# Kernel tuning notes

Measured on AMD Instinct MI355X. Metric: run time of the kernel, lower is better.

The kernel has to match this reference:

```python
import jax, jax.numpy as jnp
import numpy as np

EPS = 1e-08

def quantize_weights(w):
    # absmean ternary quantization: round(w/delta) clipped to {-1,0,1}, rescaled by delta
    delta = jnp.mean(jnp.abs(w)) + EPS
    w_quant = jnp.clip(jnp.round(w / delta), -1.0, 1.0)
    return w_quant * delta

def setup_inputs() -> dict:
    key = jax.random.key(0)
    k1, k2 = jax.random.split(key)
    B, T, IN, OUT = 8, 16, 4096, 11008
    x = jax.random.normal(k1, (B, T, IN), dtype=jnp.float32)
    weight = jax.random.normal(k2, (OUT, IN), dtype=jnp.float32)
    bias = jnp.zeros((OUT,), dtype=jnp.float32)
    return {"x": x, "weight": weight, "bias": bias}

def reference(x, weight, bias):
    w_quant = quantize_weights(weight)
    # F.linear: x @ w_quant.T + bias
    out = jnp.einsum("bti,oi->bto", x, w_quant) + bias
    return out
```

## Files before the change

### kernel.cpp

```cpp
#include <hip/hip_runtime.h>
#include <hip/hip_bf16.h>

typedef __bf16 bf16x8 __attribute__((ext_vector_type(8)));
typedef float f32x4 __attribute__((ext_vector_type(4)));
typedef unsigned short ushort8 __attribute__((ext_vector_type(8)));
typedef unsigned short ushort4v __attribute__((ext_vector_type(4)));

constexpr int M = 128;
constexpr int K = 4096;
constexpr int N = 11008;
constexpr int BN = 64;
constexpr int BK = 32;
constexpr int KSPLIT = 4;
constexpr int KBLK = K / KSPLIT;
constexpr int NBX = N / BN;
constexpr long long NW = (long long)N * K;
constexpr int RBLK = 2048;
constexpr size_t MN = (size_t)M * N;

constexpr size_t PART_OFF = 0;
constexpr size_t XBF_OFF  = 8192;
constexpr size_t P_OFF    = XBF_OFF + (size_t)M * K * 2;
constexpr size_t WS_NEED  = P_OFF + KSPLIT * MN * sizeof(float);
constexpr size_t WS_MIN   = RBLK * sizeof(float);

__device__ __forceinline__ unsigned short f2bf_bits(float f) {
    unsigned int u = __builtin_bit_cast(unsigned int, f);
    u += 0x7FFFu + ((u >> 16) & 1u);
    return (unsigned short)(u >> 16);
}

template <bool CVT>
__global__ __launch_bounds__(256) void absmean_partial(const float* __restrict__ w,
                                                       const float* __restrict__ x,
                                                       float* __restrict__ partials,
                                                       unsigned short* __restrict__ xbf)
{
    const int gtid = blockIdx.x * blockDim.x + threadIdx.x;
    if (CVT && gtid < M * K / 8) {
        const float4* xp = (const float4*)x + (size_t)gtid * 2;
        float4 a = xp[0], b = xp[1];
        ushort8 o;
        o[0] = f2bf_bits(a.x); o[1] = f2bf_bits(a.y);
        o[2] = f2bf_bits(a.z); o[3] = f2bf_bits(a.w);
        o[4] = f2bf_bits(b.x); o[5] = f2bf_bits(b.y);
        o[6] = f2bf_bits(b.z); o[7] = f2bf_bits(b.w);
        *(ushort8*)(xbf + (size_t)gtid * 8) = o;
    }
    const int n4 = (int)(NW / 4);
    const float4* w4 = (const float4*)w;
    float s0 = 0.f, s1 = 0.f, s2 = 0.f, s3 = 0.f;
    for (int i = gtid; i < n4; i += gridDim.x * blockDim.x) {
        float4 v = w4[i];
        s0 += fabsf(v.x); s1 += fabsf(v.y); s2 += fabsf(v.z); s3 += fabsf(v.w);
    }
    float s = (s0 + s1) + (s2 + s3);
#pragma unroll
    for (int off = 32; off > 0; off >>= 1) s += __shfl_down(s, off, 64);
    __shared__ float red[4];
    if ((threadIdx.x & 63) == 0) red[threadIdx.x >> 6] = s;
    __syncthreads();
    if (threadIdx.x == 0)
        partials[blockIdx.x] = (red[0] + red[1]) + (red[2] + red[3]);
}

template <int KSTEPS, bool PRE>
__global__ __launch_bounds__(256, 4) void bitlinear_gemm(
    const void* __restrict__ Xsrc, const float* __restrict__ W,
    const float* __restrict__ bias, const float* __restrict__ partials,
    float* __restrict__ dbase)
{
    constexpr int LDSW = 40;
    __shared__ __attribute__((aligned(16))) unsigned short xs[2][M * LDSW];
    __shared__ __attribute__((aligned(16))) unsigned short wsm[2][BN * LDSW];
    __shared__ float red[4];

    const int tid = threadIdx.x;
    const int lane = tid & 63;
    const int wid = tid >> 6;
    const int wm = wid >> 1;
    const int wn = wid & 1;
    const int cgrp = lane >> 4;
    const int l15 = lane & 15;
    const int n0 = blockIdx.x * BN;
    const int kk0 = PRE ? blockIdx.y * KBLK : 0;
    const int K4 = K / 4;

    const unsigned short* xb = (const unsigned short*)Xsrc;
    const float4* x4p = (const float4*)Xsrc;
    const float4* w4p = (const float4*)W;

    ushort8 xrA[2], xrB[2];
    float4 xfA[4], xfB[4];
    float4 wrA[2], wrB[2];

    auto issue_set = [&](int t, ushort8 (&xr)[2], float4 (&xf)[4], float4 (&wr)[2]) {
        if constexpr (PRE) {
#pragma unroll
            for (int i = 0; i < 2; ++i) {
                const int j = tid + i * 256;
                xr[i] = *(const ushort8*)(xb + (size_t)(j >> 2) * K + kk0 + t * BK + (j & 3) * 8);
            }
        } else {
#pragma unroll
            for (int i = 0; i < 4; ++i) {
                const int j = tid + i * 256;
                xf[i] = x4p[(size_t)(j >> 3) * K4 + (t * BK) / 4 + (j & 7)];
            }
        }
#pragma unroll
        for (int i = 0; i < 2; ++i) {
            const int j = tid + i * 256;
            wr[i] = w4p[(size_t)(n0 + (j >> 3)) * K4 + (kk0 + t * BK) / 4 + (j & 7)];
        }
    };

    float ps[RBLK / 256];
#pragma unroll
    for (int i = 0; i < RBLK / 256; ++i) ps[i] = partials[tid + i * 256];

    issue_set(0, xrA, xfA, wrA);
    if (KSTEPS > 1) issue_set(1, xrB, xfB, wrB);

    float s = 0.f;
#pragma unroll
    for (int i = 0; i < RBLK / 256; ++i) s += ps[i];
#pragma unroll
    for (int off = 32; off > 0; off >>= 1) s += __shfl_down(s, off, 64);
    if (lane == 0) red[wid] = s;
    __syncthreads();
    const float delta =
        (float)((double)((red[0] + red[1]) + (red[2] + red[3])) / (double)NW + 1e-8);
    const float inv_delta = 1.0f / delta;

    auto stage_set = [&](int buf, ushort8 (&xr)[2], float4 (&xf)[4], float4 (&wr)[2]) {
        if constexpr (PRE) {
#pragma unroll
            for (int i = 0; i < 2; ++i) {
                const int j = tid + i * 256;
                *(ushort8*)&xs[buf][(j >> 2) * LDSW + (j & 3) * 8] = xr[i];
            }
        } else {
#pragma unroll
            for (int i = 0; i < 4; ++i) {
                const int j = tid + i * 256;
                float4 v = xf[i];
                ushort4v o;
                o[0] = f2bf_bits(v.x); o[1] = f2bf_bits(v.y);
                o[2] = f2bf_bits(v.z); o[3] = f2bf_bits(v.w);
                *(ushort4v*)&xs[buf][(j >> 3) * LDSW + (j & 7) * 4] = o;
            }
        }
#pragma unroll
        for (int i = 0; i < 2; ++i) {
            const int j = tid + i * 256;
            float wf[4] = {wr[i].x, wr[i].y, wr[i].z, wr[i].w};
            ushort4v wq;
#pragma unroll
            for (int e = 0; e < 4; ++e) {
                float qv = rintf(wf[e] * inv_delta);
                qv = fminf(1.f, fmaxf(-1.f, qv));
                wq[e] = f2bf_bits(qv);
            }
            *(ushort4v*)&wsm[buf][(j >> 3) * LDSW + (j & 7) * 4] = wq;
        }
    };

    f32x4 acc[4][2] = {};

    auto compute = [&](int buf) {
        const unsigned short* xcur = xs[buf];
        const unsigned short* wcur = wsm[buf];
        bf16x8 afr[4], bfr[2];
#pragma unroll
        for (int f = 0; f < 4; ++f)
            afr[f] = *(const bf16x8*)&xcur[(wm * 64 + f * 16 + l15) * LDSW + cgrp * 8];
#pragma unroll
        for (int g = 0; g < 2; ++g)
            bfr[g] = *(const bf16x8*)&wcur[(wn * 32 + g * 16 + l15) * LDSW + cgrp * 8];
#pragma unroll
        for (int f = 0; f < 4; ++f)
#pragma unroll
            for (int g = 0; g < 2; ++g)
                acc[f][g] = __builtin_amdgcn_mfma_f32_16x16x32_bf16(
                    afr[f], bfr[g], acc[f][g], 0, 0, 0);
    };

    for (int t = 0; t < KSTEPS; t += 2) {
        stage_set(0, xrA, xfA, wrA);
        if (t + 2 < KSTEPS) issue_set(t + 2, xrA, xfA, wrA);
        __syncthreads();
        compute(0);
        stage_set(1, xrB, xfB, wrB);
        if (t + 3 < KSTEPS) issue_set(t + 3, xrB, xfB, wrB);
        __syncthreads();
        compute(1);
    }

    float* dst = PRE ? dbase + (size_t)blockIdx.y * MN : dbase;
#pragma unroll
    for (int f = 0; f < 4; ++f) {
        const int mrow = wm * 64 + f * 16 + cgrp * 4;
#pragma unroll
        for (int g = 0; g < 2; ++g) {
            const int ocol = n0 + wn * 32 + g * 16 + l15;
            const float bv = PRE ? 0.f : bias[ocol];
#pragma unroll
            for (int r = 0; r < 4; ++r)
                dst[(size_t)(mrow + r) * N + ocol] = delta * acc[f][g][r] + bv;
        }
    }
}

__global__ __launch_bounds__(256) void combine(const float* __restrict__ p,
                                               const float* __restrict__ bias,
                                               float4* __restrict__ out)
{
    const int i4 = blockIdx.x * blockDim.x + threadIdx.x;
    constexpr int N4 = N / 4;
    if (i4 >= (int)(MN / 4)) return;
    const int col4 = i4 % N4;
    float4 s = *(const float4*)(bias + col4 * 4);
#pragma unroll
    for (int y = 0; y < KSPLIT; ++y) {
        float4 v = ((const float4*)(p + y * MN))[i4];
        s.x += v.x; s.y += v.y; s.z += v.z; s.w += v.w;
    }
    out[i4] = s;
}

extern "C" void kernel_launch(void* const* d_in, const int* in_sizes, int n_in,
                              void* d_out, int out_size, void* d_ws, size_t ws_size,
                              hipStream_t stream) {
    const float* x = (const float*)d_in[0];
    const float* w = (const float*)d_in[1];
    const float* bias = (const float*)d_in[2];
    float* out = (float*)d_out;
    float* partials = (float*)((char*)d_ws + PART_OFF);
    unsigned short* xbf = (unsigned short*)((char*)d_ws + XBF_OFF);
    float* pbase = (float*)((char*)d_ws + P_OFF);

    if (ws_size >= WS_NEED) {
        absmean_partial<true><<<RBLK, 256, 0, stream>>>(w, x, partials, xbf);
        bitlinear_gemm<KBLK / BK, true><<<dim3(NBX, KSPLIT), 256, 0, stream>>>(
            xbf, w, bias, partials, pbase);
        combine<<<(int)(MN / 4 + 255) / 256, 256, 0, stream>>>(pbase, bias, (float4*)out);
    } else if (ws_size >= WS_MIN) {
        absmean_partial<false><<<RBLK, 256, 0, stream>>>(w, x, partials, xbf);
        bitlinear_gemm<K / BK, false><<<dim3(NBX, 1), 256, 0, stream>>>(
            x, w, bias, partials, out);
    }
}
```

Before: 71.67 us.

## Fuse split-K combine into GEMM via per-column-tile atomic ticket

Drops the separate combine kernel. Each split-K GEMM block takes a ticket with an atomic counter per N tile, and the last block to finish sums the partial slices plus bias into the output for that tile. This saves a kernel launch and lets the reduction overlap with other blocks' GEMM work, and the partials are more likely to still be in cache. In exchange it adds a memset launch and thread fences, and the final reduction is serialized onto one block per tile.

```diff
diff --git a/kernel.cpp b/kernel.cpp
--- a/kernel.cpp
+++ b/kernel.cpp
@@ -19,7 +19,8 @@
 constexpr size_t MN = (size_t)M * N;
 
 constexpr size_t PART_OFF = 0;
-constexpr size_t XBF_OFF  = 8192;
+constexpr size_t DONE_OFF = 8192;
+constexpr size_t XBF_OFF  = 16384;
 constexpr size_t P_OFF    = XBF_OFF + (size_t)M * K * 2;
 constexpr size_t WS_NEED  = P_OFF + KSPLIT * MN * sizeof(float);
 constexpr size_t WS_MIN   = RBLK * sizeof(float);
@@ -68,7 +69,8 @@
 __global__ __launch_bounds__(256, 4) void bitlinear_gemm(
     const void* __restrict__ Xsrc, const float* __restrict__ W,
     const float* __restrict__ bias, const float* __restrict__ partials,
-    float* __restrict__ dbase)
+    float* __restrict__ dbase, float* __restrict__ outp,
+    unsigned int* __restrict__ done)
 {
     constexpr int LDSW = 40;
     __shared__ __attribute__((aligned(16))) unsigned short xs[2][M * LDSW];
@@ -210,23 +212,30 @@
                 dst[(size_t)(mrow + r) * N + ocol] = delta * acc[f][g][r] + bv;
         }
     }
-}
-
-__global__ __launch_bounds__(256) void combine(const float* __restrict__ p,
-                                               const float* __restrict__ bias,
-                                               float4* __restrict__ out)
-{
-    const int i4 = blockIdx.x * blockDim.x + threadIdx.x;
-    constexpr int N4 = N / 4;
-    if (i4 >= (int)(MN / 4)) return;
-    const int col4 = i4 % N4;
-    float4 s = *(const float4*)(bias + col4 * 4);
-#pragma unroll
-    for (int y = 0; y < KSPLIT; ++y) {
-        float4 v = ((const float4*)(p + y * MN))[i4];
-        s.x += v.x; s.y += v.y; s.z += v.z; s.w += v.w;
-    }
-    out[i4] = s;
+
+    if constexpr (PRE) {
+        __threadfence();
+        __shared__ unsigned int ticket;
+        if (tid == 0) ticket = atomicAdd(&done[blockIdx.x], 1u);
+        __syncthreads();
+        if (ticket == KSPLIT - 1) {
+            __threadfence();
+            constexpr int N4 = N / 4, C4 = BN / 4;
+            const float4* bias4 = (const float4*)bias;
+            float4* out4 = (float4*)outp;
+            for (int j = tid; j < M * C4; j += 256) {
+                const int m = j >> 4, c = j & 15;
+                const int g4 = m * N4 + (n0 >> 2) + c;
+                float4 sv = bias4[(n0 >> 2) + c];
+#pragma unroll
+                for (int y = 0; y < KSPLIT; ++y) {
+                    float4 v = ((const float4*)(dbase + (size_t)y * MN))[g4];
+                    sv.x += v.x; sv.y += v.y; sv.z += v.z; sv.w += v.w;
+                }
+                out4[g4] = sv;
+            }
+        }
+    }
 }
 
 extern "C" void kernel_launch(void* const* d_in, const int* in_sizes, int n_in,
@@ -236,18 +245,20 @@
     const float* w = (const float*)d_in[1];
     const float* bias = (const float*)d_in[2];
     float* out = (float*)d_out;
-    float* partials = (float*)((char*)d_ws + PART_OFF);
-    unsigned short* xbf = (unsigned short*)((char*)d_ws + XBF_OFF);
-    float* pbase = (float*)((char*)d_ws + P_OFF);
+    char* wsb = (char*)d_ws;
+    float* partials = (float*)(wsb + PART_OFF);
+    unsigned int* done = (unsigned int*)(wsb + DONE_OFF);
+    unsigned short* xbf = (unsigned short*)(wsb + XBF_OFF);
+    float* pbase = (float*)(wsb + P_OFF);
 
     if (ws_size >= WS_NEED) {
+        hipMemsetAsync(done, 0, (size_t)NBX * 4, stream);
         absmean_partial<true><<<RBLK, 256, 0, stream>>>(w, x, partials, xbf);
         bitlinear_gemm<KBLK / BK, true><<<dim3(NBX, KSPLIT), 256, 0, stream>>>(
-            xbf, w, bias, partials, pbase);
-        combine<<<(int)(MN / 4 + 255) / 256, 256, 0, stream>>>(pbase, bias, (float4*)out);
+            xbf, w, bias, partials, pbase, out, done);
     } else if (ws_size >= WS_MIN) {
         absmean_partial<false><<<RBLK, 256, 0, stream>>>(w, x, partials, xbf);
         bitlinear_gemm<K / BK, false><<<dim3(NBX, 1), 256, 0, stream>>>(
-            x, w, bias, partials, out);
-    }
-}
+            x, w, bias, partials, out, out, done);
+    }
+}
```

After: 198.5 us. 177% more time.
